# Kernel optimization log

Hardware: AMD Instinct MI355X
Metric: run time of the kernel (lower is better)

## Reference

```python
import jax, jax.numpy as jnp
import numpy as np

N, L, C, KF = 32, 1024, 3, 256
H = C * KF            # hidden_dim = 768
M = 3072              # mlp_dim
EPS = 1e-6


def setup_inputs() -> dict:
    key = jax.random.key(0)
    ks = jax.random.split(key, 14)
    s = lambda fan: 1.0 / np.sqrt(fan)
    return {
        "x": jax.random.normal(ks[0], (N, L, H), dtype=jnp.float32),
        # per-channel QKV linears: Linear(k_factor, 3*k_factor) for each channel
        "W_qkv": jax.random.normal(ks[1], (C, KF, 3 * KF), dtype=jnp.float32) * s(KF),
        "b_qkv": jax.random.normal(ks[2], (C, 3 * KF), dtype=jnp.float32) * 0.01,
        "W_out": jax.random.normal(ks[3], (KF, KF), dtype=jnp.float32) * s(KF),
        "b_out": jax.random.normal(ks[4], (KF,), dtype=jnp.float32) * 0.01,
        "ln1_g": jnp.ones((H,), jnp.float32),
        "ln1_b": jnp.zeros((H,), jnp.float32),
        "ln2_g": jnp.ones((H,), jnp.float32),
        "ln2_b": jnp.zeros((H,), jnp.float32),
        "W1": jax.random.normal(ks[5], (H, M), dtype=jnp.float32) * s(H),
        "b1": jax.random.normal(ks[6], (M,), dtype=jnp.float32) * 1e-6,
        "W2": jax.random.normal(ks[7], (M, H), dtype=jnp.float32) * s(M),
        "b2": jax.random.normal(ks[8], (H,), dtype=jnp.float32) * 1e-6,
    }


def _ln(x, g, b):
    mu = jnp.mean(x, axis=-1, keepdims=True)
    var = jnp.mean(jnp.square(x - mu), axis=-1, keepdims=True)
    return (x - mu) * jax.lax.rsqrt(var + EPS) * g + b


def _criss_cross_attn(h, W_qkv, b_qkv, W_out, b_out):
    # h: [N, L, H]; hidden layout is channel-major: (C, KF)
    hc = h.reshape(h.shape[0], h.shape[1], C, KF)
    qkv = jnp.einsum("nlck,ckd->nlcd", hc, W_qkv) + b_qkv      # [N,L,C,3KF]
    q, k, v = jnp.split(qkv, 3, axis=-1)                        # each [N,L,C,KF]
    # move k_factor axis before channel axis: [N,L,KF,C]
    q = jnp.swapaxes(q, -1, -2)
    k = jnp.swapaxes(k, -1, -2)
    v = jnp.swapaxes(v, -1, -2)
    # outer-product scores over channels: [N,L,KF,C,C]
    scores = q[..., :, None] * k[..., None, :] / np.sqrt(KF)
    attn = jax.nn.softmax(scores, axis=-1)
    # einsum 'ijklm,ijkl->ijkm': sum over first channel axis
    ctx = jnp.einsum("nlkcd,nlkc->nlkd", attn, v)               # [N,L,KF,C]
    ctx = jnp.swapaxes(ctx, -1, -2)                             # [N,L,C,KF]
    out = ctx @ W_out + b_out                                   # fc_out per k_factor
    return out.reshape(h.shape[0], h.shape[1], H)


def reference(x, W_qkv, b_qkv, W_out, b_out, ln1_g, ln1_b, ln2_g, ln2_b, W1, b1, W2, b2):
    h = _ln(x, ln1_g, ln1_b)
    a = _criss_cross_attn(h, W_qkv, b_qkv, W_out, b_out)
    xr = a + x                                                   # residual (dropout=0)
    y = _ln(xr, ln2_g, ln2_b)
    y = jax.nn.gelu(y @ W1 + b1, approximate=False) @ W2 + b2    # MLPBlock
    return xr + y
```

## Files before the change

### kernel.cpp

```cpp
#include <hip/hip_runtime.h>
#include <hip/hip_bf16.h>
#include <math.h>

#define CDIV(a,b) (((a)+(b)-1)/(b))

typedef __attribute__((ext_vector_type(8))) short short8;
typedef __attribute__((ext_vector_type(4))) float f32x4;

__device__ __forceinline__ float bf2f(__hip_bfloat16 h) { return __bfloat162float(h); }
__device__ __forceinline__ __hip_bfloat16 f2bf(float f) { return __float2bfloat16(f); }

__device__ __forceinline__ float gelu_f(float v) {
  const float u = v * (0.7978845608f + 0.0356774081f * v * v);
  const float e = __expf(2.0f * u);
  const float t = 1.0f - 2.0f * __builtin_amdgcn_rcpf(e + 1.0f);
  return 0.5f * v * (1.0f + t);
}

__global__ __launch_bounds__(256) void ln_kernel(
    const float* __restrict__ in, const float* __restrict__ g,
    const float* __restrict__ b, __hip_bfloat16* __restrict__ out)
{
  __shared__ float sm1[4], sm2[4];
  const int row = blockIdx.x;
  const int tid = threadIdx.x;
  const float* p = in + (size_t)row * 768;
  float x0 = p[tid], x1 = p[tid + 256], x2 = p[tid + 512];
  float s = x0 + x1 + x2;
  #pragma unroll
  for (int off = 32; off > 0; off >>= 1) s += __shfl_down(s, off, 64);
  const int l = tid & 63, w = tid >> 6;
  if (l == 0) sm1[w] = s;
  __syncthreads();
  const float mu = (sm1[0] + sm1[1] + sm1[2] + sm1[3]) * (1.0f / 768.0f);
  const float d0 = x0 - mu, d1 = x1 - mu, d2 = x2 - mu;
  float ss = d0*d0 + d1*d1 + d2*d2;
  #pragma unroll
  for (int off = 32; off > 0; off >>= 1) ss += __shfl_down(ss, off, 64);
  if (l == 0) sm2[w] = ss;
  __syncthreads();
  const float var = (sm2[0] + sm2[1] + sm2[2] + sm2[3]) * (1.0f / 768.0f);
  const float rstd = rsqrtf(var + 1e-6f);
  __hip_bfloat16* q = out + (size_t)row * 768;
  q[tid]       = f2bf(d0 * rstd * g[tid]       + b[tid]);
  q[tid + 256] = f2bf(d1 * rstd * g[tid + 256] + b[tid + 256]);
  q[tid + 512] = f2bf(d2 * rstd * g[tid + 512] + b[tid + 512]);
}

__global__ __launch_bounds__(256) void attn_kernel(
    const __hip_bfloat162* __restrict__ qkv, __hip_bfloat162* __restrict__ ctx)
{
  const long t = (long)blockIdx.x * 256 + threadIdx.x;
  const long row = t >> 7;
  const int kp = (int)(t & 127);
  const __hip_bfloat162* p = qkv + row * 1152;
  float q[3][2], k[3][2], v[3][2];
  #pragma unroll
  for (int c = 0; c < 3; ++c) {
    __hip_bfloat162 qq = p[c*384 + kp];
    __hip_bfloat162 kk = p[c*384 + 128 + kp];
    __hip_bfloat162 vv = p[c*384 + 256 + kp];
    q[c][0] = __low2float(qq); q[c][1] = __high2float(qq);
    k[c][0] = __low2float(kk); k[c][1] = __high2float(kk);
    v[c][0] = __low2float(vv); v[c][1] = __high2float(vv);
  }
  float o[3][2] = {};
  #pragma unroll
  for (int u = 0; u < 2; ++u) {
    #pragma unroll
    for (int c = 0; c < 3; ++c) {
      const float s0 = q[c][u]*k[0][u]*0.0625f, s1 = q[c][u]*k[1][u]*0.0625f, s2 = q[c][u]*k[2][u]*0.0625f;
      const float m = fmaxf(s0, fmaxf(s1, s2));
      const float e0 = __expf(s0-m), e1 = __expf(s1-m), e2 = __expf(s2-m);
      const float inv = v[c][u] / (e0 + e1 + e2);
      o[0][u] += e0*inv; o[1][u] += e1*inv; o[2][u] += e2*inv;
    }
  }
  __hip_bfloat162* po = ctx + row * 384;
  #pragma unroll
  for (int d = 0; d < 3; ++d)
    po[d*128 + kp] = __hip_bfloat162{f2bf(o[d][0]), f2bf(o[d][1])};
}

__global__ __launch_bounds__(256) void transpose_bf16_kernel(
    const float* __restrict__ in, __hip_bfloat16* __restrict__ out, int K, int N)
{
  __shared__ float tile[32][33];
  in  += (size_t)blockIdx.z * K * N;
  out += (size_t)blockIdx.z * K * N;
  const int n0 = blockIdx.x * 32;
  const int k0 = blockIdx.y * 32;
  const int tx = threadIdx.x & 31, ty = threadIdx.x >> 5;
  #pragma unroll
  for (int r = 0; r < 32; r += 8)
    tile[ty + r][tx] = in[(size_t)(k0 + ty + r) * N + n0 + tx];
  __syncthreads();
  #pragma unroll
  for (int r = 0; r < 32; r += 8)
    out[(size_t)(n0 + ty + r) * K + k0 + tx] = f2bf(tile[tx][ty + r]);
}

#define BM 128
#define BN 128
#define BK 32

template<int MODE>
__global__ __launch_bounds__(256) void gemm_bt_kernel(
    const __hip_bfloat16* __restrict__ A, int lda, long strideA,
    const __hip_bfloat16* __restrict__ Bt, int ldb, long strideB,
    float* __restrict__ Cf, __hip_bfloat16* __restrict__ Cb, int ldc, long strideC,
    const float* __restrict__ bias, long strideBias,
    const float* __restrict__ res,
    int K)
{
  __shared__ __align__(16) char sAll[2 * 16384];

  const int z = blockIdx.z;
  A    += (size_t)z * strideA;
  Bt   += (size_t)z * strideB;
  bias += (size_t)z * strideBias;
  const long cOff = (long)z * strideC;

  const long tileM = (long)blockIdx.x * BM;
  const int  tileN = blockIdx.y * BN;

  const int tid  = threadIdx.x;
  const int lane = tid & 63;
  const int wv   = tid >> 6;
  const int waveM = (wv & 1) * 64;
  const int waveN = (wv >> 1) * 64;

  const int srow  = tid >> 2;
  const int selem = ((tid & 3) ^ ((srow >> 1) & 3)) * 8;
  const int frow = lane & 15;
  const int fkb  = (((lane >> 4) ^ ((frow >> 1) & 3)) << 4);

  const __hip_bfloat16* Ab = A  + tileM * (size_t)lda + selem;
  const __hip_bfloat16* Bb = Bt + (long)tileN * (size_t)ldb + selem;

  f32x4 acc[4][4] = {};

  const int T = K / BK;

  {
    #pragma unroll
    for (int hh = 0; hh < 2; ++hh) {
      const int r = hh * 64 + srow;
      __builtin_amdgcn_global_load_lds(
          (const __attribute__((address_space(1))) void*)(Ab + (size_t)r * lda),
          (__attribute__((address_space(3))) void*)(sAll + hh*4096 + tid*16), 16, 0, 0);
      __builtin_amdgcn_global_load_lds(
          (const __attribute__((address_space(1))) void*)(Bb + (size_t)r * ldb),
          (__attribute__((address_space(3))) void*)(sAll + 8192 + hh*4096 + tid*16), 16, 0, 0);
    }
  }

  for (int t = 0; t < T; ++t) {
    const int buf = (t & 1) * 16384;
    if (t + 1 < T) {
      const int nbuf = 16384 - buf;
      const int k0 = (t + 1) * BK;
      #pragma unroll
      for (int hh = 0; hh < 2; ++hh) {
        const int r = hh * 64 + srow;
        __builtin_amdgcn_global_load_lds(
            (const __attribute__((address_space(1))) void*)(Ab + (size_t)r * lda + k0),
            (__attribute__((address_space(3))) void*)(sAll + nbuf + hh*4096 + tid*16), 16, 0, 0);
        __builtin_amdgcn_global_load_lds(
            (const __attribute__((address_space(1))) void*)(Bb + (size_t)r * ldb + k0),
            (__attribute__((address_space(3))) void*)(sAll + nbuf + 8192 + hh*4096 + tid*16), 16, 0, 0);
      }
      asm volatile("s_waitcnt vmcnt(4)" ::: "memory");
    } else {
      asm volatile("s_waitcnt vmcnt(0)" ::: "memory");
    }
    __builtin_amdgcn_s_barrier();

    const char* sAb = sAll + buf;
    const char* sBb = sAb + 8192;
    short8 aF[4], bF[4];
    #pragma unroll
    for (int i = 0; i < 4; ++i)
      aF[i] = *(const short8*)(sAb + (waveM + i*16 + frow) * 64 + fkb);
    #pragma unroll
    for (int j = 0; j < 4; ++j)
      bF[j] = *(const short8*)(sBb + (waveN + j*16 + frow) * 64 + fkb);
    #pragma unroll
    for (int i = 0; i < 4; ++i)
      #pragma unroll
      for (int j = 0; j < 4; ++j)
        acc[i][j] = __builtin_amdgcn_mfma_f32_16x16x32_bf16(aF[i], bF[j], acc[i][j], 0, 0, 0);

    __builtin_amdgcn_s_barrier();
  }

  #pragma unroll
  for (int i = 0; i < 4; ++i) {
    const long row0 = tileM + waveM + i*16 + ((lane >> 4) * 4);
    #pragma unroll
    for (int j = 0; j < 4; ++j) {
      const int col = tileN + waveN + j*16 + (lane & 15);
      const float bv = bias[col];
      #pragma unroll
      for (int r = 0; r < 4; ++r) {
        const long idx = cOff + (row0 + r) * (long)ldc + col;
        const float v = acc[i][j][r] + bv;
        if (MODE == 0) {
          Cb[idx] = f2bf(v);
        } else if (MODE == 1 || MODE == 3) {
          Cf[idx] = v + res[idx];
        } else {
          Cb[idx] = f2bf(gelu_f(v));
        }
      }
    }
  }
}

extern "C" void kernel_launch(void* const* d_in, const int* in_sizes, int n_in,
                              void* d_out, int out_size, void* d_ws, size_t ws_size,
                              hipStream_t stream)
{
  const float* x     = (const float*)d_in[0];
  const float* W_qkv = (const float*)d_in[1];
  const float* b_qkv = (const float*)d_in[2];
  const float* W_out = (const float*)d_in[3];
  const float* b_out = (const float*)d_in[4];
  const float* ln1_g = (const float*)d_in[5];
  const float* ln1_b = (const float*)d_in[6];
  const float* ln2_g = (const float*)d_in[7];
  const float* ln2_b = (const float*)d_in[8];
  const float* W1    = (const float*)d_in[9];
  const float* b1    = (const float*)d_in[10];
  const float* W2    = (const float*)d_in[11];
  const float* b2    = (const float*)d_in[12];
  float* out = (float*)d_out;

  char* ws = (char*)d_ws;
  __hip_bfloat16* h     = (__hip_bfloat16*)(ws + 0);
  __hip_bfloat16* qkv   = (__hip_bfloat16*)(ws + 50331648);
  __hip_bfloat16* ctx   = (__hip_bfloat16*)(ws + 0);
  __hip_bfloat16* act   = (__hip_bfloat16*)(ws + 0);
  __hip_bfloat16* yln   = (__hip_bfloat16*)(ws + 201326592);
  __hip_bfloat16* wqkvT = (__hip_bfloat16*)(ws + 251658240);
  __hip_bfloat16* woutT = (__hip_bfloat16*)(ws + 252837888);
  __hip_bfloat16* w1T   = (__hip_bfloat16*)(ws + 252968960);
  __hip_bfloat16* w2T   = (__hip_bfloat16*)(ws + 257687552);

  transpose_bf16_kernel<<<dim3(768/32, 256/32, 3), 256, 0, stream>>>(W_qkv, wqkvT, 256, 768);
  transpose_bf16_kernel<<<dim3(256/32, 256/32, 1), 256, 0, stream>>>(W_out, woutT, 256, 256);
  transpose_bf16_kernel<<<dim3(3072/32, 768/32, 1), 256, 0, stream>>>(W1, w1T, 768, 3072);
  transpose_bf16_kernel<<<dim3(768/32, 3072/32, 1), 256, 0, stream>>>(W2, w2T, 3072, 768);

  ln_kernel<<<32768, 256, 0, stream>>>(x, ln1_g, ln1_b, h);

  gemm_bt_kernel<0><<<dim3(32768/BM, 768/BN, 3), 256, 0, stream>>>(
      h, 768, 256, wqkvT, 256, 768*256, nullptr, qkv, 2304, 768, b_qkv, 768, nullptr, 256);

  attn_kernel<<<16384, 256, 0, stream>>>((const __hip_bfloat162*)qkv, (__hip_bfloat162*)ctx);

  gemm_bt_kernel<1><<<dim3(98304/BM, 256/BN, 1), 256, 0, stream>>>(
      ctx, 256, 0, woutT, 256, 0, out, nullptr, 256, 0, b_out, 0, x, 256);

  ln_kernel<<<32768, 256, 0, stream>>>(out, ln2_g, ln2_b, yln);

  gemm_bt_kernel<2><<<dim3(32768/BM, 3072/BN, 1), 256, 0, stream>>>(
      yln, 768, 0, w1T, 768, 0, nullptr, act, 3072, 0, b1, 0, nullptr, 768);

  gemm_bt_kernel<3><<<dim3(32768/BM, 768/BN, 1), 256, 0, stream>>>(
      act, 3072, 0, w2T, 3072, 0, out, nullptr, 768, 0, b2, 0, out, 3072);
}
```

Before: 893.4 us.

## Add 256x256-tile GEMM with direct global-to-LDS loads and interleaved pipeline

Adds a new GEMM kernel that uses 256x256 output tiles computed by 512 threads. It stages operands into double-buffered, XOR-swizzled LDS with global_load_lds and splits each k-step into four quarter-tile MFMA phases, each overlapped with the next stage's loads and tuned with wait counts and priority hints. The QKV, MLP-up and MLP-down GEMMs now use it, aiming for more data reuse per tile and better overlap of memory traffic with compute. In exchange it uses 128 KB of LDS per block and many more accumulator registers, and it assumes M and N divide by 256 and K by 64.

```diff
diff --git a/kernel.cpp b/kernel.cpp
--- a/kernel.cpp
+++ b/kernel.cpp
@@ -1,8 +1,6 @@
 #include <hip/hip_runtime.h>
 #include <hip/hip_bf16.h>
 #include <math.h>
-
-#define CDIV(a,b) (((a)+(b)-1)/(b))
 
 typedef __attribute__((ext_vector_type(8))) short short8;
 typedef __attribute__((ext_vector_type(4))) float f32x4;
@@ -215,6 +213,183 @@
       }
     }
   }
+}
+
+#define GLL16(src, dst) __builtin_amdgcn_global_load_lds( \
+    (const __attribute__((address_space(1))) void*)(src), \
+    (__attribute__((address_space(3))) void*)(dst), 16, 0, 0)
+
+#define STAGE_A(h, bufo, koff) do { \
+    GLL16(Ab + (size_t)((h)*128 + 0) * lda + (koff), sAll + (bufo) + (h)*16384 + 0*8192 + tid*16); \
+    GLL16(Ab + (size_t)((h)*128 + 64) * lda + (koff), sAll + (bufo) + (h)*16384 + 1*8192 + tid*16); \
+  } while (0)
+#define STAGE_B(h, bufo, koff) do { \
+    GLL16(Bb + (size_t)((h)*128 + 0) * ldb + (koff), sAll + (bufo) + 32768 + (h)*16384 + 0*8192 + tid*16); \
+    GLL16(Bb + (size_t)((h)*128 + 64) * ldb + (koff), sAll + (bufo) + 32768 + (h)*16384 + 1*8192 + tid*16); \
+  } while (0)
+
+template<int MODE>
+__global__ __launch_bounds__(512, 2) void gemm256_kernel(
+    const __hip_bfloat16* __restrict__ A, int lda, long strideA,
+    const __hip_bfloat16* __restrict__ Bt, int ldb, long strideB,
+    float* __restrict__ Cf, __hip_bfloat16* __restrict__ Cb, int ldc, long strideC,
+    const float* __restrict__ bias, long strideBias,
+    const float* __restrict__ res,
+    int K)
+{
+  __shared__ __align__(16) char sAll[2 * 65536];
+
+  const int z = blockIdx.z;
+  A    += (size_t)z * strideA;
+  Bt   += (size_t)z * strideB;
+  bias += (size_t)z * strideBias;
+  const long cOff = (long)z * strideC;
+
+  const long tileM = (long)blockIdx.x * 256;
+  const int  tileN = blockIdx.y * 256;
+
+  const int tid  = threadIdx.x;
+  const int lane = tid & 63;
+  const int wv   = tid >> 6;
+  const int wm   = wv & 1;
+  const int wn   = wv >> 1;
+
+  const int srow  = tid >> 3;
+  const int selem = ((tid & 7) ^ (srow & 7)) * 8;
+
+  const __hip_bfloat16* Ab = A  + (tileM + srow) * (size_t)lda + selem;
+  const __hip_bfloat16* Bb = Bt + ((long)tileN + srow) * (size_t)ldb + selem;
+
+  const int fk   = lane >> 4;
+  const int fx   = lane & 7;
+  const int arow = (wm*64 + (lane & 15)) * 128;
+  const int brow = (wn*32 + (lane & 15)) * 128;
+  const int ax0  = ((0*4 + fk) ^ fx) * 16;
+  const int ax1  = ((1*4 + fk) ^ fx) * 16;
+
+  f32x4 acc[2][2][4][2] = {};
+  const int T = K / 64;
+
+  STAGE_A(0, 0, 0);
+  STAGE_B(0, 0, 0);
+  STAGE_B(1, 0, 0);
+  STAGE_A(1, 0, 0);
+
+  for (int t = 0; t < T; ++t) {
+    const int buf  = (t & 1) * 65536;
+    const int nbuf = 65536 - buf;
+    const int kn   = ((t + 1 < T) ? (t + 1) : t) * 64;
+
+    short8 aF[4][2], bF0[2][2], bF1[2][2];
+
+    asm volatile("s_waitcnt vmcnt(4)" ::: "memory");
+    __builtin_amdgcn_s_barrier();
+    STAGE_A(0, nbuf, kn);
+    {
+      const char* sA = sAll + buf;
+      const char* sB = sAll + buf + 32768;
+      #pragma unroll
+      for (int i = 0; i < 4; ++i) {
+        aF[i][0] = *(const short8*)(sA + arow + i*2048 + ax0);
+        aF[i][1] = *(const short8*)(sA + arow + i*2048 + ax1);
+      }
+      #pragma unroll
+      for (int j = 0; j < 2; ++j) {
+        bF0[j][0] = *(const short8*)(sB + brow + j*2048 + ax0);
+        bF0[j][1] = *(const short8*)(sB + brow + j*2048 + ax1);
+      }
+    }
+    __builtin_amdgcn_s_setprio(1);
+    #pragma unroll
+    for (int i = 0; i < 4; ++i)
+      #pragma unroll
+      for (int j = 0; j < 2; ++j) {
+        acc[0][0][i][j] = __builtin_amdgcn_mfma_f32_16x16x32_bf16(aF[i][0], bF0[j][0], acc[0][0][i][j], 0, 0, 0);
+        acc[0][0][i][j] = __builtin_amdgcn_mfma_f32_16x16x32_bf16(aF[i][1], bF0[j][1], acc[0][0][i][j], 0, 0, 0);
+      }
+    __builtin_amdgcn_s_setprio(0);
+
+    STAGE_B(0, nbuf, kn);
+    asm volatile("s_waitcnt vmcnt(6)" ::: "memory");
+    __builtin_amdgcn_s_barrier();
+    {
+      const char* sB = sAll + buf + 32768 + 16384;
+      #pragma unroll
+      for (int j = 0; j < 2; ++j) {
+        bF1[j][0] = *(const short8*)(sB + brow + j*2048 + ax0);
+        bF1[j][1] = *(const short8*)(sB + brow + j*2048 + ax1);
+      }
+    }
+    __builtin_amdgcn_s_setprio(1);
+    #pragma unroll
+    for (int i = 0; i < 4; ++i)
+      #pragma unroll
+      for (int j = 0; j < 2; ++j) {
+        acc[0][1][i][j] = __builtin_amdgcn_mfma_f32_16x16x32_bf16(aF[i][0], bF1[j][0], acc[0][1][i][j], 0, 0, 0);
+        acc[0][1][i][j] = __builtin_amdgcn_mfma_f32_16x16x32_bf16(aF[i][1], bF1[j][1], acc[0][1][i][j], 0, 0, 0);
+      }
+    __builtin_amdgcn_s_setprio(0);
+
+    STAGE_B(1, nbuf, kn);
+    asm volatile("s_waitcnt vmcnt(6)" ::: "memory");
+    __builtin_amdgcn_s_barrier();
+    {
+      const char* sA = sAll + buf + 16384;
+      #pragma unroll
+      for (int i = 0; i < 4; ++i) {
+        aF[i][0] = *(const short8*)(sA + arow + i*2048 + ax0);
+        aF[i][1] = *(const short8*)(sA + arow + i*2048 + ax1);
+      }
+    }
+    __builtin_amdgcn_s_setprio(1);
+    #pragma unroll
+    for (int i = 0; i < 4; ++i)
+      #pragma unroll
+      for (int j = 0; j < 2; ++j) {
+        acc[1][1][i][j] = __builtin_amdgcn_mfma_f32_16x16x32_bf16(aF[i][0], bF1[j][0], acc[1][1][i][j], 0, 0, 0);
+        acc[1][1][i][j] = __builtin_amdgcn_mfma_f32_16x16x32_bf16(aF[i][1], bF1[j][1], acc[1][1][i][j], 0, 0, 0);
+      }
+    __builtin_amdgcn_s_setprio(0);
+
+    STAGE_A(1, nbuf, kn);
+    __builtin_amdgcn_s_setprio(1);
+    #pragma unroll
+    for (int i = 0; i < 4; ++i)
+      #pragma unroll
+      for (int j = 0; j < 2; ++j) {
+        acc[1][0][i][j] = __builtin_amdgcn_mfma_f32_16x16x32_bf16(aF[i][0], bF0[j][0], acc[1][0][i][j], 0, 0, 0);
+        acc[1][0][i][j] = __builtin_amdgcn_mfma_f32_16x16x32_bf16(aF[i][1], bF0[j][1], acc[1][0][i][j], 0, 0, 0);
+      }
+    __builtin_amdgcn_s_setprio(0);
+  }
+
+  asm volatile("s_waitcnt vmcnt(0)" ::: "memory");
+
+  #pragma unroll
+  for (int ih = 0; ih < 2; ++ih)
+    #pragma unroll
+    for (int jh = 0; jh < 2; ++jh)
+      #pragma unroll
+      for (int i = 0; i < 4; ++i) {
+        const long row0 = tileM + ih*128 + wm*64 + i*16 + ((lane >> 4) * 4);
+        #pragma unroll
+        for (int j = 0; j < 2; ++j) {
+          const int col = tileN + jh*128 + wn*32 + j*16 + (lane & 15);
+          const float bv = bias[col];
+          #pragma unroll
+          for (int r = 0; r < 4; ++r) {
+            const long idx = cOff + (row0 + r) * (long)ldc + col;
+            const float v = acc[ih][jh][i][j][r] + bv;
+            if (MODE == 0) {
+              Cb[idx] = f2bf(v);
+            } else if (MODE == 1 || MODE == 3) {
+              Cf[idx] = v + res[idx];
+            } else {
+              Cb[idx] = f2bf(gelu_f(v));
+            }
+          }
+        }
+      }
 }
 
 extern "C" void kernel_launch(void* const* d_in, const int* in_sizes, int n_in,
@@ -254,7 +429,7 @@
 
   ln_kernel<<<32768, 256, 0, stream>>>(x, ln1_g, ln1_b, h);
 
-  gemm_bt_kernel<0><<<dim3(32768/BM, 768/BN, 3), 256, 0, stream>>>(
+  gemm256_kernel<0><<<dim3(32768/256, 768/256, 3), 512, 0, stream>>>(
       h, 768, 256, wqkvT, 256, 768*256, nullptr, qkv, 2304, 768, b_qkv, 768, nullptr, 256);
 
   attn_kernel<<<16384, 256, 0, stream>>>((const __hip_bfloat162*)qkv, (__hip_bfloat162*)ctx);
@@ -264,9 +439,9 @@
 
   ln_kernel<<<32768, 256, 0, stream>>>(out, ln2_g, ln2_b, yln);
 
-  gemm_bt_kernel<2><<<dim3(32768/BM, 3072/BN, 1), 256, 0, stream>>>(
+  gemm256_kernel<2><<<dim3(32768/256, 3072/256, 1), 512, 0, stream>>>(
       yln, 768, 0, w1T, 768, 0, nullptr, act, 3072, 0, b1, 0, nullptr, 768);
 
-  gemm_bt_kernel<3><<<dim3(32768/BM, 768/BN, 1), 256, 0, stream>>>(
+  gemm256_kernel<3><<<dim3(32768/256, 768/256, 1), 512, 0, stream>>>(
       act, 3072, 0, w2T, 3072, 0, out, nullptr, 768, 0, b2, 0, out, 3072);
 }
```

After: 787.2 us. -11.9%, faster.

## Add triple-buffered 256x128 GEMM kernel with swizzled LDS for QKV and MLP

Applied to the files above, without the earlier changes.

Adds a new GEMM kernel with a 256x128 tile, 512 threads (8 waves), BK=64 and three LDS stages loaded through global_load_lds. An XOR swizzle on the LDS layout avoids bank conflicts, and split lgkmcnt waits interleave fragment reads with MFMA, using s_setprio around the MFMA blocks. The QKV, MLP1 and MLP2 GEMMs now use it. The aim is to hide global-load latency better and raise data reuse per tile, at the cost of 144KB of LDS per block, which limits occupancy.

```diff
diff --git a/kernel.cpp b/kernel.cpp
--- a/kernel.cpp
+++ b/kernel.cpp
@@ -1,8 +1,6 @@
 #include <hip/hip_runtime.h>
 #include <hip/hip_bf16.h>
 #include <math.h>
-
-#define CDIV(a,b) (((a)+(b)-1)/(b))
 
 typedef __attribute__((ext_vector_type(8))) short short8;
 typedef __attribute__((ext_vector_type(4))) float f32x4;
@@ -175,6 +173,7 @@
       asm volatile("s_waitcnt vmcnt(0)" ::: "memory");
     }
     __builtin_amdgcn_s_barrier();
+    asm volatile("" ::: "memory");
 
     const char* sAb = sAll + buf;
     const char* sBb = sAb + 8192;
@@ -200,6 +199,136 @@
     #pragma unroll
     for (int j = 0; j < 4; ++j) {
       const int col = tileN + waveN + j*16 + (lane & 15);
+      const float bv = bias[col];
+      #pragma unroll
+      for (int r = 0; r < 4; ++r) {
+        const long idx = cOff + (row0 + r) * (long)ldc + col;
+        const float v = acc[i][j][r] + bv;
+        if (MODE == 0) {
+          Cb[idx] = f2bf(v);
+        } else if (MODE == 1 || MODE == 3) {
+          Cf[idx] = v + res[idx];
+        } else {
+          Cb[idx] = f2bf(gelu_f(v));
+        }
+      }
+    }
+  }
+}
+
+#define GLL16(src, dst) __builtin_amdgcn_global_load_lds( \
+    (const __attribute__((address_space(1))) void*)(src), \
+    (__attribute__((address_space(3))) void*)(dst), 16, 0, 0)
+
+#define STAGE_TILE3(bb, koff) do { \
+    char* bse = sAll + (bb) * 49152; \
+    GLL16(Ab + (size_t)(0*64) * lda + (koff), bse + 0*8192  + tid*16); \
+    GLL16(Ab + (size_t)(1*64) * lda + (koff), bse + 1*8192  + tid*16); \
+    GLL16(Ab + (size_t)(2*64) * lda + (koff), bse + 2*8192  + tid*16); \
+    GLL16(Ab + (size_t)(3*64) * lda + (koff), bse + 3*8192  + tid*16); \
+    GLL16(Bb + (size_t)(0*64) * ldb + (koff), bse + 32768 + 0*8192 + tid*16); \
+    GLL16(Bb + (size_t)(1*64) * ldb + (koff), bse + 32768 + 1*8192 + tid*16); \
+  } while (0)
+
+template<int MODE>
+__global__ __launch_bounds__(512, 2) void gemm3_kernel(
+    const __hip_bfloat16* __restrict__ A, int lda, long strideA,
+    const __hip_bfloat16* __restrict__ Bt, int ldb, long strideB,
+    float* __restrict__ Cf, __hip_bfloat16* __restrict__ Cb, int ldc, long strideC,
+    const float* __restrict__ bias, long strideBias,
+    const float* __restrict__ res,
+    int K)
+{
+  __shared__ __align__(16) char sAll[3 * 49152];
+
+  const int z = blockIdx.z;
+  A    += (size_t)z * strideA;
+  Bt   += (size_t)z * strideB;
+  bias += (size_t)z * strideBias;
+  const long cOff = (long)z * strideC;
+
+  const long tileM = (long)blockIdx.x * 256;
+  const int  tileN = blockIdx.y * 128;
+
+  const int tid  = threadIdx.x;
+  const int lane = tid & 63;
+  const int wv   = tid >> 6;
+  const int wm   = wv & 3;
+  const int wn   = wv >> 2;
+
+  const int srow  = tid >> 3;
+  const int selem = ((tid & 7) ^ (srow & 7)) * 8;
+
+  const __hip_bfloat16* Ab = A  + (tileM + srow) * (size_t)lda + selem;
+  const __hip_bfloat16* Bb = Bt + ((long)tileN + srow) * (size_t)ldb + selem;
+
+  const int fk   = lane >> 4;
+  const int fx   = lane & 7;
+  const int frow = lane & 15;
+  const int arow = (wm*64 + frow) * 128;
+  const int brow = 32768 + (wn*64 + frow) * 128;
+  const int ax0  = ((0*4 + fk) ^ fx) * 16;
+  const int ax1  = ((1*4 + fk) ^ fx) * 16;
+
+  f32x4 acc[4][4] = {};
+  const int T = K / 64;
+
+  STAGE_TILE3(0, 0);
+  STAGE_TILE3(1, (T > 1 ? 1 : 0) * 64);
+
+  int bcur = 0;
+  for (int t = 0; t < T; ++t) {
+    const char* base = sAll + bcur * 49152;
+    const int bstg = (bcur == 0) ? 2 : (bcur - 1);
+    const int kn   = (t + 2 < T ? t + 2 : T - 1) * 64;
+
+    asm volatile("s_waitcnt vmcnt(6)" ::: "memory");
+    __builtin_amdgcn_s_barrier();
+    asm volatile("" ::: "memory");
+
+    STAGE_TILE3(bstg, kn);
+
+    short8 aF0[4], bF0[4], aF1[4], bF1[4];
+    #pragma unroll
+    for (int i = 0; i < 4; ++i) aF0[i] = *(const short8*)(base + arow + i*2048 + ax0);
+    #pragma unroll
+    for (int j = 0; j < 4; ++j) bF0[j] = *(const short8*)(base + brow + j*2048 + ax0);
+    #pragma unroll
+    for (int i = 0; i < 4; ++i) aF1[i] = *(const short8*)(base + arow + i*2048 + ax1);
+    #pragma unroll
+    for (int j = 0; j < 4; ++j) bF1[j] = *(const short8*)(base + brow + j*2048 + ax1);
+
+    asm volatile("s_waitcnt lgkmcnt(8)" ::: "memory");
+    __builtin_amdgcn_sched_barrier(0);
+    __builtin_amdgcn_s_setprio(1);
+    #pragma unroll
+    for (int i = 0; i < 4; ++i)
+      #pragma unroll
+      for (int j = 0; j < 4; ++j)
+        acc[i][j] = __builtin_amdgcn_mfma_f32_16x16x32_bf16(aF0[i], bF0[j], acc[i][j], 0, 0, 0);
+    __builtin_amdgcn_s_setprio(0);
+
+    asm volatile("s_waitcnt lgkmcnt(0)" ::: "memory");
+    __builtin_amdgcn_sched_barrier(0);
+    __builtin_amdgcn_s_setprio(1);
+    #pragma unroll
+    for (int i = 0; i < 4; ++i)
+      #pragma unroll
+      for (int j = 0; j < 4; ++j)
+        acc[i][j] = __builtin_amdgcn_mfma_f32_16x16x32_bf16(aF1[i], bF1[j], acc[i][j], 0, 0, 0);
+    __builtin_amdgcn_s_setprio(0);
+
+    bcur = (bcur == 2) ? 0 : (bcur + 1);
+  }
+
+  asm volatile("s_waitcnt vmcnt(0)" ::: "memory");
+
+  #pragma unroll
+  for (int i = 0; i < 4; ++i) {
+    const long row0 = tileM + wm*64 + i*16 + ((lane >> 4) * 4);
+    #pragma unroll
+    for (int j = 0; j < 4; ++j) {
+      const int col = tileN + wn*64 + j*16 + (lane & 15);
       const float bv = bias[col];
       #pragma unroll
       for (int r = 0; r < 4; ++r) {
@@ -254,7 +383,7 @@
 
   ln_kernel<<<32768, 256, 0, stream>>>(x, ln1_g, ln1_b, h);
 
-  gemm_bt_kernel<0><<<dim3(32768/BM, 768/BN, 3), 256, 0, stream>>>(
+  gemm3_kernel<0><<<dim3(32768/256, 768/128, 3), 512, 0, stream>>>(
       h, 768, 256, wqkvT, 256, 768*256, nullptr, qkv, 2304, 768, b_qkv, 768, nullptr, 256);
 
   attn_kernel<<<16384, 256, 0, stream>>>((const __hip_bfloat162*)qkv, (__hip_bfloat162*)ctx);
@@ -264,9 +393,9 @@
 
   ln_kernel<<<32768, 256, 0, stream>>>(out, ln2_g, ln2_b, yln);
 
-  gemm_bt_kernel<2><<<dim3(32768/BM, 3072/BN, 1), 256, 0, stream>>>(
+  gemm3_kernel<2><<<dim3(32768/256, 3072/128, 1), 512, 0, stream>>>(
       yln, 768, 0, w1T, 768, 0, nullptr, act, 3072, 0, b1, 0, nullptr, 768);
 
-  gemm_bt_kernel<3><<<dim3(32768/BM, 768/BN, 1), 256, 0, stream>>>(
+  gemm3_kernel<3><<<dim3(32768/256, 768/128, 1), 512, 0, stream>>>(
       act, 3072, 0, w2T, 3072, 0, out, nullptr, 768, 0, b2, 0, out, 3072);
 }
```

New measurement: 855.5 us. 1.04x faster.
